# Kernel optimization log

Hardware: AMD Instinct MI355X
Metric: run time of the kernel (lower is better)

## Reference

```python
import jax, jax.numpy as jnp
import numpy as np

B, L, D_IN, D_H = 8, 16384, 256, 256  # leaves L = 2**14, complete binary tree
N = 2 * L - 1  # total nodes, heap layout: children of j are 2j+1, 2j+2


def setup_inputs() -> dict:
    key = jax.random.key(0)
    ks = jax.random.split(key, 7)
    s_in = 1.0 / float(np.sqrt(D_IN))
    s_h = 1.0 / float(np.sqrt(D_H))
    return {
        "x": jax.random.normal(ks[0], (B, N, D_IN), jnp.float32),
        "W_iou": jax.random.uniform(ks[1], (D_IN, 3 * D_H), jnp.float32, -s_in, s_in),
        "b_iou": jax.random.uniform(ks[2], (3 * D_H,), jnp.float32, -s_in, s_in),
        "U_iou": jax.random.uniform(ks[3], (D_H, 3 * D_H), jnp.float32, -s_h, s_h),
        "W_f": jax.random.uniform(ks[4], (D_IN, D_H), jnp.float32, -s_in, s_in),
        "b_f": jax.random.uniform(ks[5], (D_IN,)[:0] + (D_H,), jnp.float32, -s_in, s_in),
        "U_f": jax.random.uniform(ks[6], (D_H, D_H), jnp.float32, -s_h, s_h),
    }


def reference(x, W_iou, b_iou, U_iou, W_f, b_f, U_f):
    Bn, Nn, _ = x.shape
    H = U_f.shape[0]
    Lv = (Nn + 1) // 2  # number of leaves
    depth = int(np.log2(Lv))

    # --- leaf nodes (no children): heap indices Lv-1 .. 2Lv-2 ---
    x_leaf = x[:, Lv - 1:, :]                       # [B, L, d_in]
    iou = x_leaf @ W_iou + b_iou                    # [B, L, 3H]
    i, o, u = jnp.split(iou, 3, axis=-1)
    c = jax.nn.sigmoid(i) * jnp.tanh(u)
    h = jax.nn.sigmoid(o) * jnp.tanh(c)             # [B, L, H]

    # --- internal levels, bottom-up; each node has exactly 2 children ---
    n = Lv
    for _ in range(depth):
        n //= 2
        x_lvl = x[:, n - 1:2 * n - 1, :]            # [B, n, d_in]
        hc = h.reshape(Bn, n, 2, H)                 # children hidden states
        cc = c.reshape(Bn, n, 2, H)                 # children cell states
        h_sum = hc.sum(axis=2)                      # child-sum  [B, n, H]
        iou = x_lvl @ W_iou + b_iou + h_sum @ U_iou
        i, o, u = jnp.split(iou, 3, axis=-1)
        # per-child forget gate: sigmoid(W_f x + b_f + U_f h_j)
        f = jax.nn.sigmoid((x_lvl @ W_f + b_f)[:, :, None, :]
                           + jnp.einsum('bnch,hk->bnck', hc, U_f))
        c = jax.nn.sigmoid(i) * jnp.tanh(u) + (f * cc).sum(axis=2)
        h = jax.nn.sigmoid(o) * jnp.tanh(c)

    # root h, c concatenated -> [B, 2H]
    return jnp.concatenate([h[:, 0, :], c[:, 0, :]], axis=-1)
```

## Files before the change

### kernel.cpp

```cpp
#include <hip/hip_runtime.h>
#include <math.h>


#define Bb 8
#define Lleaf 16384
#define Nn 32767
#define Dd 256

typedef __attribute__((ext_vector_type(8))) short short8;
typedef __attribute__((ext_vector_type(4))) float float4v;

__device__ __forceinline__ float sigf(float x) {
    return __builtin_amdgcn_rcpf(1.0f + __expf(-x));
}
__device__ __forceinline__ float tanh_fast(float x) {
    return fmaf(2.0f, sigf(2.0f * x), -1.0f);
}
__device__ __forceinline__ unsigned short f2bf(float f) {
    unsigned int u = __float_as_uint(f);
    u = (u + 0x7FFFu + ((u >> 16) & 1u)) >> 16;
    return (unsigned short)u;
}
__device__ __forceinline__ float bf2f(unsigned short h) {
    return __uint_as_float(((unsigned int)h) << 16);
}
__device__ __forceinline__ void load_lds16(const void* g, void* l) {
    __builtin_amdgcn_global_load_lds(
        (const __attribute__((address_space(1))) unsigned int*)g,
        (__attribute__((address_space(3))) unsigned int*)l, 16, 0, 0);
}

__global__ __launch_bounds__(256) void xcast(
    const float* __restrict__ x, unsigned short* __restrict__ xbf)
{
    const int base = (blockIdx.x * 256 + threadIdx.x) * 8;
    const float4* p = (const float4*)(x + base);
    const float4 f0 = p[0], f1 = p[1];
    union { unsigned short us[8]; uint4 v; } pk;
    pk.us[0] = f2bf(f0.x); pk.us[1] = f2bf(f0.y);
    pk.us[2] = f2bf(f0.z); pk.us[3] = f2bf(f0.w);
    pk.us[4] = f2bf(f1.x); pk.us[5] = f2bf(f1.y);
    pk.us[6] = f2bf(f1.z); pk.us[7] = f2bf(f1.w);
    *(uint4*)(xbf + base) = pk.v;
}

__global__ __launch_bounds__(256) void pack_internal(
    const float* __restrict__ W_iou, const float* __restrict__ U_iou,
    const float* __restrict__ W_f,   const float* __restrict__ U_f,
    unsigned short* __restrict__ Bt)
{
    const int idx = blockIdx.x * 256 + threadIdx.x;
    const int col = idx / 768, k = idx - col * 768;
    const int q = col / 80, rem = col - q * 80;
    const int g = rem >> 4, r = rem & 15;
    const int d = (q << 4) + r;
    const int seg = k >> 8, kk = k & 255;
    float val;
    if (g < 3) {
        val = (seg == 0) ? W_iou[kk * 768 + g * 256 + d]
                         : U_iou[kk * 768 + g * 256 + d];
    } else if (seg == 0) {
        val = W_f[kk * 256 + d];
    } else if (seg == 1) {
        val = (g == 3) ? U_f[kk * 256 + d] : 0.0f;
    } else {
        val = (g == 4) ? U_f[kk * 256 + d] : 0.0f;
    }
    Bt[idx] = f2bf(val);
}

__global__ __launch_bounds__(256) void pack_leaf(
    const float* __restrict__ W_iou, unsigned short* __restrict__ Btl)
{
    const int idx = blockIdx.x * 256 + threadIdx.x;
    const int col = idx >> 8, k = idx & 255;
    const int q = col / 48, rem = col - q * 48;
    const int g = rem >> 4, r = rem & 15;
    const int d = (q << 4) + r;
    Btl[idx] = f2bf(W_iou[k * 768 + g * 256 + d]);
}

__global__ __launch_bounds__(256, 2) void gemm_level_big(
    const unsigned short* __restrict__ xbf, const unsigned short* __restrict__ Bt,
    const float* __restrict__ b_iou, const float* __restrict__ b_f,
    unsigned short* __restrict__ h_out, float* __restrict__ c_out,
    const unsigned short* __restrict__ h_ch, const float* __restrict__ c_ch,
    int n, int lvl)
{
    __shared__ unsigned short Alds[2][128 * 64];
    __shared__ unsigned short Blds[2][160 * 64];
    const int tid  = threadIdx.x;
    const int wave = tid >> 6, lane = tid & 63;
    const int l16  = lane & 15, q4 = lane >> 4;
    const int bx   = blockIdx.x >> 3, by = blockIdx.x & 7;
    const int m0   = bx * 128;
    const int n0   = by * 160;
    const int lr   = lane >> 3;
    const int lp   = (lane & 7) ^ lr;

    const int b   = m0 >> lvl;
    const int xr0 = m0 + (n - 1) + b * (Nn - n);

    auto stageA = [&](int kk, unsigned short* dst) {
        #pragma unroll
        for (int it = 0; it < 4; ++it) {
            const int g = it * 4 + wave;
            const int r = g * 8 + lr;
            const unsigned short* src;
            if (kk < 4) {
                src = xbf + (((xr0 + r) << 8) + kk * 64 + lp * 8);
            } else {
                const int sel = (kk >= 8) ? 1 : 0;
                src = h_ch + (((2 * (m0 + r) + sel) << 8) + ((kk - 4) & 3) * 64 + lp * 8);
            }
            load_lds16(src, dst + g * 512);
        }
    };
    auto stageB = [&](int kk, unsigned short* dst) {
        #pragma unroll
        for (int it = 0; it < 5; ++it) {
            const int g = it * 4 + wave;
            const int row = g * 8 + lr;
            load_lds16(Bt + ((n0 + row) * 768 + kk * 64 + lp * 8), dst + g * 512);
        }
    };

    unsigned short* Ac = Alds[0]; unsigned short* An = Alds[1];
    unsigned short* Bc = Blds[0]; unsigned short* Bn = Blds[1];

    stageA(0, Ac); stageB(0, Bc);

    float4v acc[2][10];
    #pragma unroll
    for (int qq = 0; qq < 2; ++qq) {
        const int d = ((by * 2 + qq) << 4) + l16;
        float bv0 = b_iou[d], bv1 = b_iou[256 + d], bv2 = b_iou[512 + d];
        float bv3 = b_f[d];
        float bv[5] = {bv0, bv1, bv2, bv3, bv3};
        #pragma unroll
        for (int g = 0; g < 5; ++g) {
            float4v v; v[0] = bv[g]; v[1] = bv[g]; v[2] = bv[g]; v[3] = bv[g];
            acc[0][qq * 5 + g] = v; acc[1][qq * 5 + g] = v;
        }
    }

    asm volatile("s_waitcnt vmcnt(0)" ::: "memory");
    __builtin_amdgcn_s_barrier();

    for (int kk = 0; kk < 12; ++kk) {
        if (kk < 11) { stageA(kk + 1, An); stageB(kk + 1, Bn); }
        #pragma unroll
        for (int ks = 0; ks < 2; ++ks) {
            const int pa = ks * 4 + q4;
            const int sw = (pa ^ (l16 & 7)) * 8;
            const short8 a0 = *(const short8*)&Ac[(wave * 32 + l16) * 64 + sw];
            const short8 a1 = *(const short8*)&Ac[(wave * 32 + 16 + l16) * 64 + sw];
            #pragma unroll
            for (int ni = 0; ni < 10; ++ni) {
                const short8 bf = *(const short8*)&Bc[(ni * 16 + l16) * 64 + sw];
                acc[0][ni] = __builtin_amdgcn_mfma_f32_16x16x32_bf16(a0, bf, acc[0][ni], 0, 0, 0);
                acc[1][ni] = __builtin_amdgcn_mfma_f32_16x16x32_bf16(a1, bf, acc[1][ni], 0, 0, 0);
            }
        }
        if (kk < 11) {
            asm volatile("s_waitcnt vmcnt(0)" ::: "memory");
            __builtin_amdgcn_s_barrier();
            unsigned short* t = Ac; Ac = An; An = t;
            t = Bc; Bc = Bn; Bn = t;
        }
    }

    #pragma unroll
    for (int mi = 0; mi < 2; ++mi) {
        #pragma unroll
        for (int reg = 0; reg < 4; ++reg) {
            const int row_l = wave * 32 + mi * 16 + (q4 << 2) + reg;
            const int m = m0 + row_l;
            const int cbase = (2 * m) << 8;
            const int obase = m << 8;
            #pragma unroll
            for (int qq = 0; qq < 2; ++qq) {
                const int d = ((by * 2 + qq) << 4) + l16;
                const float i_ = acc[mi][qq * 5 + 0][reg];
                const float o_ = acc[mi][qq * 5 + 1][reg];
                const float u_ = acc[mi][qq * 5 + 2][reg];
                const float f1 = acc[mi][qq * 5 + 3][reg];
                const float f2 = acc[mi][qq * 5 + 4][reg];
                const float c1 = c_ch[cbase + d];
                const float c2 = c_ch[cbase + 256 + d];
                const float c = sigf(i_) * tanh_fast(u_) + sigf(f1) * c1 + sigf(f2) * c2;
                const float h = sigf(o_) * tanh_fast(c);
                c_out[obase + d] = c;
                h_out[obase + d] = f2bf(h);
            }
        }
    }
}

__global__ __launch_bounds__(256, 2) void gemm_level(
    const unsigned short* __restrict__ xbf, const unsigned short* __restrict__ Bt,
    const float* __restrict__ b_iou, const float* __restrict__ b_f,
    unsigned short* __restrict__ h_out, float* __restrict__ c_out,
    const unsigned short* __restrict__ h_ch, const float* __restrict__ c_ch,
    int n, int lvl)
{
    __shared__ unsigned short Alds[2][128 * 64];
    __shared__ unsigned short Blds[2][160 * 64];
    const int tid  = threadIdx.x;
    const int wave = tid >> 6, lane = tid & 63;
    const int l16  = lane & 15, q4 = lane >> 4;
    const int m0   = blockIdx.x * 128;
    const int n0   = blockIdx.y * 160;
    const int lr   = lane >> 3;
    const int lp   = (lane & 7) ^ lr;

    auto stageA = [&](int kk, unsigned short* dst) {
        #pragma unroll
        for (int it = 0; it < 4; ++it) {
            const int g = it * 4 + wave;
            const int r = g * 8 + lr;
            const int m = m0 + r;
            const unsigned short* src;
            if (kk < 4) {
                const int bb = m >> lvl;
                src = xbf + (((m + (n - 1) + bb * (Nn - n)) << 8) + kk * 64 + lp * 8);
            } else {
                const int sel = (kk >= 8) ? 1 : 0;
                src = h_ch + (((2 * m + sel) << 8) + ((kk - 4) & 3) * 64 + lp * 8);
            }
            load_lds16(src, dst + g * 512);
        }
    };
    auto stageB = [&](int kk, unsigned short* dst) {
        #pragma unroll
        for (int it = 0; it < 5; ++it) {
            const int g = it * 4 + wave;
            const int row = g * 8 + lr;
            load_lds16(Bt + ((n0 + row) * 768 + kk * 64 + lp * 8), dst + g * 512);
        }
    };

    unsigned short* Ac = Alds[0]; unsigned short* An = Alds[1];
    unsigned short* Bc = Blds[0]; unsigned short* Bn = Blds[1];

    stageA(0, Ac); stageB(0, Bc);

    float4v acc[2][10];
    #pragma unroll
    for (int qq = 0; qq < 2; ++qq) {
        const int d = ((blockIdx.y * 2 + qq) << 4) + l16;
        float bv0 = b_iou[d], bv1 = b_iou[256 + d], bv2 = b_iou[512 + d];
        float bv3 = b_f[d];
        float bv[5] = {bv0, bv1, bv2, bv3, bv3};
        #pragma unroll
        for (int g = 0; g < 5; ++g) {
            float4v v; v[0] = bv[g]; v[1] = bv[g]; v[2] = bv[g]; v[3] = bv[g];
            acc[0][qq * 5 + g] = v; acc[1][qq * 5 + g] = v;
        }
    }

    asm volatile("s_waitcnt vmcnt(0)" ::: "memory");
    __builtin_amdgcn_s_barrier();

    for (int kk = 0; kk < 12; ++kk) {
        if (kk < 11) { stageA(kk + 1, An); stageB(kk + 1, Bn); }
        #pragma unroll
        for (int ks = 0; ks < 2; ++ks) {
            const int pa = ks * 4 + q4;
            const int sw = (pa ^ (l16 & 7)) * 8;
            const short8 a0 = *(const short8*)&Ac[(wave * 32 + l16) * 64 + sw];
            const short8 a1 = *(const short8*)&Ac[(wave * 32 + 16 + l16) * 64 + sw];
            #pragma unroll
            for (int ni = 0; ni < 10; ++ni) {
                const short8 bf = *(const short8*)&Bc[(ni * 16 + l16) * 64 + sw];
                acc[0][ni] = __builtin_amdgcn_mfma_f32_16x16x32_bf16(a0, bf, acc[0][ni], 0, 0, 0);
                acc[1][ni] = __builtin_amdgcn_mfma_f32_16x16x32_bf16(a1, bf, acc[1][ni], 0, 0, 0);
            }
        }
        if (kk < 11) {
            asm volatile("s_waitcnt vmcnt(0)" ::: "memory");
            __builtin_amdgcn_s_barrier();
            unsigned short* t = Ac; Ac = An; An = t;
            t = Bc; Bc = Bn; Bn = t;
        }
    }

    #pragma unroll
    for (int mi = 0; mi < 2; ++mi) {
        #pragma unroll
        for (int reg = 0; reg < 4; ++reg) {
            const int row_l = wave * 32 + mi * 16 + (q4 << 2) + reg;
            const int m = m0 + row_l;
            const int cbase = (2 * m) << 8;
            const int obase = m << 8;
            #pragma unroll
            for (int qq = 0; qq < 2; ++qq) {
                const int d = ((blockIdx.y * 2 + qq) << 4) + l16;
                const float i_ = acc[mi][qq * 5 + 0][reg];
                const float o_ = acc[mi][qq * 5 + 1][reg];
                const float u_ = acc[mi][qq * 5 + 2][reg];
                const float f1 = acc[mi][qq * 5 + 3][reg];
                const float f2 = acc[mi][qq * 5 + 4][reg];
                const float c1 = c_ch[cbase + d];
                const float c2 = c_ch[cbase + 256 + d];
                const float c = sigf(i_) * tanh_fast(u_) + sigf(f1) * c1 + sigf(f2) * c2;
                const float h = sigf(o_) * tanh_fast(c);
                c_out[obase + d] = c;
                h_out[obase + d] = f2bf(h);
            }
        }
    }
}

__global__ __launch_bounds__(256, 2) void gemm_small(
    const unsigned short* __restrict__ xbf, const unsigned short* __restrict__ Bt,
    const float* __restrict__ b_iou, const float* __restrict__ b_f,
    unsigned short* __restrict__ h_out, float* __restrict__ c_out,
    const unsigned short* __restrict__ h_ch, const float* __restrict__ c_ch,
    int n, int lvl)
{
    __shared__ unsigned short Alds[2][64 * 64];
    __shared__ unsigned short Blds[2][160 * 64];
    const int tid  = threadIdx.x;
    const int wave = tid >> 6, lane = tid & 63;
    const int l16  = lane & 15, q4 = lane >> 4;
    const int n0   = blockIdx.y * 160;
    const int lr   = lane >> 3;
    const int lp   = (lane & 7) ^ lr;
    const int rmax = 8 * n - 1;

    auto stageA = [&](int kk, unsigned short* dst) {
        #pragma unroll
        for (int it = 0; it < 2; ++it) {
            const int g = it * 4 + wave;
            const int r = g * 8 + lr;
            const int m = (r > rmax) ? rmax : r;
            const unsigned short* src;
            if (kk < 4) {
                const int bb = m >> lvl;
                src = xbf + (((m + (n - 1) + bb * (Nn - n)) << 8) + kk * 64 + lp * 8);
            } else {
                const int sel = (kk >= 8) ? 1 : 0;
                src = h_ch + (((2 * m + sel) << 8) + ((kk - 4) & 3) * 64 + lp * 8);
            }
            load_lds16(src, dst + g * 512);
        }
    };
    auto stageB = [&](int kk, unsigned short* dst) {
        #pragma unroll
        for (int it = 0; it < 5; ++it) {
            const int g = it * 4 + wave;
            const int row = g * 8 + lr;
            load_lds16(Bt + ((n0 + row) * 768 + kk * 64 + lp * 8), dst + g * 512);
        }
    };

    unsigned short* Ac = Alds[0]; unsigned short* An = Alds[1];
    unsigned short* Bc = Blds[0]; unsigned short* Bn = Blds[1];

    stageA(0, Ac); stageB(0, Bc);

    float4v acc[10];
    #pragma unroll
    for (int qq = 0; qq < 2; ++qq) {
        const int d = ((blockIdx.y * 2 + qq) << 4) + l16;
        float bv0 = b_iou[d], bv1 = b_iou[256 + d], bv2 = b_iou[512 + d];
        float bv3 = b_f[d];
        float bv[5] = {bv0, bv1, bv2, bv3, bv3};
        #pragma unroll
        for (int g = 0; g < 5; ++g) {
            float4v v; v[0] = bv[g]; v[1] = bv[g]; v[2] = bv[g]; v[3] = bv[g];
            acc[qq * 5 + g] = v;
        }
    }

    asm volatile("s_waitcnt vmcnt(0)" ::: "memory");
    __builtin_amdgcn_s_barrier();

    for (int kk = 0; kk < 12; ++kk) {
        if (kk < 11) { stageA(kk + 1, An); stageB(kk + 1, Bn); }
        #pragma unroll
        for (int ks = 0; ks < 2; ++ks) {
            const int pa = ks * 4 + q4;
            const int sw = (pa ^ (l16 & 7)) * 8;
            const short8 a0 = *(const short8*)&Ac[(wave * 16 + l16) * 64 + sw];
            #pragma unroll
            for (int ni = 0; ni < 10; ++ni) {
                const short8 bf = *(const short8*)&Bc[(ni * 16 + l16) * 64 + sw];
                acc[ni] = __builtin_amdgcn_mfma_f32_16x16x32_bf16(a0, bf, acc[ni], 0, 0, 0);
            }
        }
        if (kk < 11) {
            asm volatile("s_waitcnt vmcnt(0)" ::: "memory");
            __builtin_amdgcn_s_barrier();
            unsigned short* t = Ac; Ac = An; An = t;
            t = Bc; Bc = Bn; Bn = t;
        }
    }

    #pragma unroll
    for (int reg = 0; reg < 4; ++reg) {
        const int row_l = wave * 16 + (q4 << 2) + reg;
        const int m = (row_l > rmax) ? rmax : row_l;
        const bool valid = (row_l <= rmax);
        const int cbase = (2 * m) << 8;
        const int obase = m << 8;
        #pragma unroll
        for (int qq = 0; qq < 2; ++qq) {
            const int d = ((blockIdx.y * 2 + qq) << 4) + l16;
            const float i_ = acc[qq * 5 + 0][reg];
            const float o_ = acc[qq * 5 + 1][reg];
            const float u_ = acc[qq * 5 + 2][reg];
            const float f1 = acc[qq * 5 + 3][reg];
            const float f2 = acc[qq * 5 + 4][reg];
            const float c1 = c_ch[cbase + d];
            const float c2 = c_ch[cbase + 256 + d];
            const float c = sigf(i_) * tanh_fast(u_) + sigf(f1) * c1 + sigf(f2) * c2;
            const float h = sigf(o_) * tanh_fast(c);
            if (valid) {
                c_out[obase + d] = c;
                h_out[obase + d] = f2bf(h);
            }
        }
    }
}

__global__ __launch_bounds__(256, 2) void gemm_leaf(
    const unsigned short* __restrict__ xbf, const unsigned short* __restrict__ Btl,
    const float* __restrict__ b_iou,
    unsigned short* __restrict__ h_out, float* __restrict__ c_out)
{
    __shared__ unsigned short Alds[2][128 * 64];
    __shared__ unsigned short Blds[2][96 * 64];
    const int tid  = threadIdx.x;
    const int wave = tid >> 6, lane = tid & 63;
    const int l16  = lane & 15, q4 = lane >> 4;
    const int bx   = blockIdx.x >> 3, by = blockIdx.x & 7;
    const int m0   = bx * 128;
    const int n0   = by * 96;
    const int lr   = lane >> 3;
    const int lp   = (lane & 7) ^ lr;

    const int b   = m0 >> 14;
    const int xr0 = m0 + (Lleaf - 1) + b * (Nn - Lleaf);

    auto stageA = [&](int kk, unsigned short* dst) {
        #pragma unroll
        for (int it = 0; it < 4; ++it) {
            const int g = it * 4 + wave;
            const int r = g * 8 + lr;
            load_lds16(xbf + (((xr0 + r) << 8) + kk * 64 + lp * 8), dst + g * 512);
        }
    };
    auto stageB = [&](int kk, unsigned short* dst) {
        #pragma unroll
        for (int it = 0; it < 3; ++it) {
            const int g = it * 4 + wave;
            const int row = g * 8 + lr;
            load_lds16(Btl + ((n0 + row) * 256 + kk * 64 + lp * 8), dst + g * 512);
        }
    };

    unsigned short* Ac = Alds[0]; unsigned short* An = Alds[1];
    unsigned short* Bc = Blds[0]; unsigned short* Bn = Blds[1];

    stageA(0, Ac); stageB(0, Bc);

    float4v acc[2][6];
    #pragma unroll
    for (int qq = 0; qq < 2; ++qq) {
        const int d = ((by * 2 + qq) << 4) + l16;
        float bv[3] = {b_iou[d], b_iou[256 + d], b_iou[512 + d]};
        #pragma unroll
        for (int g = 0; g < 3; ++g) {
            float4v v; v[0] = bv[g]; v[1] = bv[g]; v[2] = bv[g]; v[3] = bv[g];
            acc[0][qq * 3 + g] = v; acc[1][qq * 3 + g] = v;
        }
    }

    asm volatile("s_waitcnt vmcnt(0)" ::: "memory");
    __builtin_amdgcn_s_barrier();

    for (int kk = 0; kk < 4; ++kk) {
        if (kk < 3) { stageA(kk + 1, An); stageB(kk + 1, Bn); }
        #pragma unroll
        for (int ks = 0; ks < 2; ++ks) {
            const int pa = ks * 4 + q4;
            const int sw = (pa ^ (l16 & 7)) * 8;
            const short8 a0 = *(const short8*)&Ac[(wave * 32 + l16) * 64 + sw];
            const short8 a1 = *(const short8*)&Ac[(wave * 32 + 16 + l16) * 64 + sw];
            #pragma unroll
            for (int ni = 0; ni < 6; ++ni) {
                const short8 bf = *(const short8*)&Bc[(ni * 16 + l16) * 64 + sw];
                acc[0][ni] = __builtin_amdgcn_mfma_f32_16x16x32_bf16(a0, bf, acc[0][ni], 0, 0, 0);
                acc[1][ni] = __builtin_amdgcn_mfma_f32_16x16x32_bf16(a1, bf, acc[1][ni], 0, 0, 0);
            }
        }
        if (kk < 3) {
            asm volatile("s_waitcnt vmcnt(0)" ::: "memory");
            __builtin_amdgcn_s_barrier();
            unsigned short* t = Ac; Ac = An; An = t;
            t = Bc; Bc = Bn; Bn = t;
        }
    }

    #pragma unroll
    for (int mi = 0; mi < 2; ++mi) {
        #pragma unroll
        for (int reg = 0; reg < 4; ++reg) {
            const int row_l = wave * 32 + mi * 16 + (q4 << 2) + reg;
            const int obase = (m0 + row_l) << 8;
            #pragma unroll
            for (int qq = 0; qq < 2; ++qq) {
                const int d = ((by * 2 + qq) << 4) + l16;
                const float i_ = acc[mi][qq * 3 + 0][reg];
                const float o_ = acc[mi][qq * 3 + 1][reg];
                const float u_ = acc[mi][qq * 3 + 2][reg];
                const float c = sigf(i_) * tanh_fast(u_);
                const float h = sigf(o_) * tanh_fast(c);
                c_out[obase + d] = c;
                h_out[obase + d] = f2bf(h);
            }
        }
    }
}

__global__ __launch_bounds__(256) void out_kernel(
    const unsigned short* __restrict__ h_root, const float* __restrict__ c_root,
    float* __restrict__ out)
{
    const int t = threadIdx.x;
    const int b = blockIdx.x;
    out[b * 512 + t]       = bf2f(h_root[(b << 8) + t]);
    out[b * 512 + 256 + t] = c_root[(b << 8) + t];
}

extern "C" void kernel_launch(void* const* d_in, const int* in_sizes, int n_in,
                              void* d_out, int out_size, void* d_ws, size_t ws_size,
                              hipStream_t stream) {
    const float* x     = (const float*)d_in[0];
    const float* W_iou = (const float*)d_in[1];
    const float* b_iou = (const float*)d_in[2];
    const float* U_iou = (const float*)d_in[3];
    const float* W_f   = (const float*)d_in[4];
    const float* b_f   = (const float*)d_in[5];
    const float* U_f   = (const float*)d_in[6];
    float* out = (float*)d_out;

    char* p = (char*)d_ws;
    unsigned short* xbf = (unsigned short*)p;  p += (size_t)Bb * Nn * Dd * 2;
    float* cE = (float*)p;                     p += (size_t)Bb * Lleaf * Dd * 4;
    float* cO = (float*)p;                     p += (size_t)Bb * (Lleaf/2) * Dd * 4;
    unsigned short* hE = (unsigned short*)p;   p += (size_t)Bb * Lleaf * Dd * 2;
    unsigned short* hO = (unsigned short*)p;   p += (size_t)Bb * (Lleaf/2) * Dd * 2;
    unsigned short* Bt  = (unsigned short*)p;  p += 1280 * 768 * 2;
    unsigned short* Btl = (unsigned short*)p;

    xcast<<<(Bb * Nn * Dd) / (256 * 8), 256, 0, stream>>>(x, xbf);
    pack_internal<<<(1280 * 768) / 256, 256, 0, stream>>>(W_iou, U_iou, W_f, U_f, Bt);
    pack_leaf<<<(768 * 256) / 256, 256, 0, stream>>>(W_iou, Btl);

    gemm_leaf<<<(Bb * Lleaf / 128) * 8, 256, 0, stream>>>(xbf, Btl, b_iou, hE, cE);

    for (int lvl = 13; lvl >= 7; --lvl) {
        const int n = 1 << lvl;
        unsigned short* ho = (lvl & 1) ? hO : hE;  float* co = (lvl & 1) ? cO : cE;
        unsigned short* hc = (lvl & 1) ? hE : hO;  float* cc = (lvl & 1) ? cE : cO;
        gemm_level_big<<<(Bb * n / 128) * 8, 256, 0, stream>>>(
            xbf, Bt, b_iou, b_f, ho, co, hc, cc, n, lvl);
    }
    for (int lvl = 6; lvl >= 4; --lvl) {
        const int n = 1 << lvl;
        unsigned short* ho = (lvl & 1) ? hO : hE;  float* co = (lvl & 1) ? cO : cE;
        unsigned short* hc = (lvl & 1) ? hE : hO;  float* cc = (lvl & 1) ? cE : cO;
        gemm_level<<<dim3(Bb * n / 128, 8), 256, 0, stream>>>(
            xbf, Bt, b_iou, b_f, ho, co, hc, cc, n, lvl);
    }
    for (int lvl = 3; lvl >= 0; --lvl) {
        const int n = 1 << lvl;
        unsigned short* ho = (lvl & 1) ? hO : hE;  float* co = (lvl & 1) ? cO : cE;
        unsigned short* hc = (lvl & 1) ? hE : hO;  float* cc = (lvl & 1) ? cE : cO;
        gemm_small<<<dim3(1, 8), 256, 0, stream>>>(
            xbf, Bt, b_iou, b_f, ho, co, hc, cc, n, lvl);
    }
    out_kernel<<<Bb, 256, 0, stream>>>(hE, cE, out);
}
```

Measured before the change: 997.8 us.

## Halve N-tile in big level GEMM and remap blocks per XCD

Result: no change. 1.013 ms (+1.6%).

```diff
diff --git a/kernel.cpp b/kernel.cpp
--- a/kernel.cpp
+++ b/kernel.cpp
@@ -80,7 +80,7 @@
     Btl[idx] = f2bf(W_iou[k * 768 + g * 256 + d]);
 }
 
-__global__ __launch_bounds__(256, 2) void gemm_level_big(
+__global__ __launch_bounds__(256, 3) void gemm_level_big(
     const unsigned short* __restrict__ xbf, const unsigned short* __restrict__ Bt,
     const float* __restrict__ b_iou, const float* __restrict__ b_f,
     unsigned short* __restrict__ h_out, float* __restrict__ c_out,
@@ -88,13 +88,21 @@
     int n, int lvl)
 {
     __shared__ unsigned short Alds[2][128 * 64];
-    __shared__ unsigned short Blds[2][160 * 64];
+    __shared__ unsigned short Blds[2][80 * 64];
     const int tid  = threadIdx.x;
     const int wave = tid >> 6, lane = tid & 63;
     const int l16  = lane & 15, q4 = lane >> 4;
-    const int bx   = blockIdx.x >> 3, by = blockIdx.x & 7;
+
+    const int p     = blockIdx.x;
+    const int xcd   = p & 7;
+    const int local = p >> 3;
+    const int by    = local & 15;
+    const int bxl   = local >> 4;
+    const int gpx   = n >> 7;
+    const int bx    = xcd * gpx + bxl;
+
     const int m0   = bx * 128;
-    const int n0   = by * 160;
+    const int n0   = by * 80;
     const int lr   = lane >> 3;
     const int lp   = (lane & 7) ^ lr;
 
@@ -118,10 +126,12 @@
     };
     auto stageB = [&](int kk, unsigned short* dst) {
         #pragma unroll
-        for (int it = 0; it < 5; ++it) {
-            const int g = it * 4 + wave;
-            const int row = g * 8 + lr;
-            load_lds16(Bt + ((n0 + row) * 768 + kk * 64 + lp * 8), dst + g * 512);
+        for (int it = 0; it < 3; ++it) {
+            const int g = it * 4 + wave;
+            if (g < 10) {
+                const int row = g * 8 + lr;
+                load_lds16(Bt + ((n0 + row) * 768 + kk * 64 + lp * 8), dst + g * 512);
+            }
         }
     };
 
@@ -130,17 +140,15 @@
 
     stageA(0, Ac); stageB(0, Bc);
 
-    float4v acc[2][10];
-    #pragma unroll
-    for (int qq = 0; qq < 2; ++qq) {
-        const int d = ((by * 2 + qq) << 4) + l16;
-        float bv0 = b_iou[d], bv1 = b_iou[256 + d], bv2 = b_iou[512 + d];
-        float bv3 = b_f[d];
-        float bv[5] = {bv0, bv1, bv2, bv3, bv3};
+    float4v acc[2][5];
+    {
+        const int d = (by << 4) + l16;
+        const float bv[5] = {b_iou[d], b_iou[256 + d], b_iou[512 + d],
+                             b_f[d], b_f[d]};
         #pragma unroll
         for (int g = 0; g < 5; ++g) {
             float4v v; v[0] = bv[g]; v[1] = bv[g]; v[2] = bv[g]; v[3] = bv[g];
-            acc[0][qq * 5 + g] = v; acc[1][qq * 5 + g] = v;
+            acc[0][g] = v; acc[1][g] = v;
         }
     }
 
@@ -156,7 +164,7 @@
             const short8 a0 = *(const short8*)&Ac[(wave * 32 + l16) * 64 + sw];
             const short8 a1 = *(const short8*)&Ac[(wave * 32 + 16 + l16) * 64 + sw];
             #pragma unroll
-            for (int ni = 0; ni < 10; ++ni) {
+            for (int ni = 0; ni < 5; ++ni) {
                 const short8 bf = *(const short8*)&Bc[(ni * 16 + l16) * 64 + sw];
                 acc[0][ni] = __builtin_amdgcn_mfma_f32_16x16x32_bf16(a0, bf, acc[0][ni], 0, 0, 0);
                 acc[1][ni] = __builtin_amdgcn_mfma_f32_16x16x32_bf16(a1, bf, acc[1][ni], 0, 0, 0);
@@ -178,21 +186,18 @@
             const int m = m0 + row_l;
             const int cbase = (2 * m) << 8;
             const int obase = m << 8;
-            #pragma unroll
-            for (int qq = 0; qq < 2; ++qq) {
-                const int d = ((by * 2 + qq) << 4) + l16;
-                const float i_ = acc[mi][qq * 5 + 0][reg];
-                const float o_ = acc[mi][qq * 5 + 1][reg];
-                const float u_ = acc[mi][qq * 5 + 2][reg];
-                const float f1 = acc[mi][qq * 5 + 3][reg];
-                const float f2 = acc[mi][qq * 5 + 4][reg];
-                const float c1 = c_ch[cbase + d];
-                const float c2 = c_ch[cbase + 256 + d];
-                const float c = sigf(i_) * tanh_fast(u_) + sigf(f1) * c1 + sigf(f2) * c2;
-                const float h = sigf(o_) * tanh_fast(c);
-                c_out[obase + d] = c;
-                h_out[obase + d] = f2bf(h);
-            }
+            const int d = (by << 4) + l16;
+            const float i_ = acc[mi][0][reg];
+            const float o_ = acc[mi][1][reg];
+            const float u_ = acc[mi][2][reg];
+            const float f1 = acc[mi][3][reg];
+            const float f2 = acc[mi][4][reg];
+            const float c1 = c_ch[cbase + d];
+            const float c2 = c_ch[cbase + 256 + d];
+            const float c = sigf(i_) * tanh_fast(u_) + sigf(f1) * c1 + sigf(f2) * c2;
+            const float h = sigf(o_) * tanh_fast(c);
+            c_out[obase + d] = c;
+            h_out[obase + d] = f2bf(h);
         }
     }
 }
@@ -435,7 +440,13 @@
     const int tid  = threadIdx.x;
     const int wave = tid >> 6, lane = tid & 63;
     const int l16  = lane & 15, q4 = lane >> 4;
-    const int bx   = blockIdx.x >> 3, by = blockIdx.x & 7;
+
+    const int p     = blockIdx.x;
+    const int xcd   = p & 7;
+    const int local = p >> 3;
+    const int by    = local & 7;
+    const int bx    = xcd * 128 + (local >> 3);
+
     const int m0   = bx * 128;
     const int n0   = by * 96;
     const int lr   = lane >> 3;
@@ -566,7 +577,7 @@
         const int n = 1 << lvl;
         unsigned short* ho = (lvl & 1) ? hO : hE;  float* co = (lvl & 1) ? cO : cE;
         unsigned short* hc = (lvl & 1) ? hE : hO;  float* cc = (lvl & 1) ? cE : cO;
-        gemm_level_big<<<(Bb * n / 128) * 8, 256, 0, stream>>>(
+        gemm_level_big<<<(Bb * n / 128) * 16, 256, 0, stream>>>(
             xbf, Bt, b_iou, b_f, ho, co, hc, cc, n, lvl);
     }
     for (int lvl = 6; lvl >= 4; --lvl) {
```
